# Optimization experiments

Hardware: AMD Instinct MI355X
Metric: run time of the kernel (lower is better)

Reference implementation:

```python
import jax, jax.numpy as jnp
import numpy as np


def _eta(pos, conj):
    # e[0] = pos[:,1::2] repeated into even/odd cols; e[1] = (+/-)pos[:,0::2] likewise
    c = jnp.repeat(pos[:, 1::2], 2, axis=1)
    s = jnp.repeat(pos[:, 0::2], 2, axis=1)
    return jnp.stack([c, s if conj else -s])  # [2, N, d]


def setup_inputs() -> dict:
    key = jax.random.key(0)
    ks = jax.random.split(key, 8)
    B, N, d, H = 8, 4096, 128, 4
    s = 0.02
    return {
        "x": jax.random.normal(ks[0], (B, N, d), jnp.float32),
        "pos": jax.random.normal(ks[1], (N, d), jnp.float32),
        "W_lt": jax.random.normal(ks[2], (d, d), jnp.float32) * s,
        "W_phi": jax.random.normal(ks[3], (d * H, d), jnp.float32) * s,
        "b_phi": jnp.zeros((d * H,), jnp.float32),
        "W_c1": jax.random.normal(ks[4], (H, H), jnp.float32) * s,
        "b_c1": jnp.zeros((H,), jnp.float32),
        "W_c2": jax.random.normal(ks[5], (1, H), jnp.float32) * s,
        "b_c2": jnp.zeros((1,), jnp.float32),
        "ln_g": jnp.ones((d,), jnp.float32),
        "ln_b": jnp.zeros((d,), jnp.float32),
        "W_f1": jax.random.normal(ks[6], (d, d), jnp.float32) * s,
        "b_f1": jnp.zeros((d,), jnp.float32),
        "W_f2": jax.random.normal(ks[7], (d, d), jnp.float32) * s,
        "b_f2": jnp.zeros((d,), jnp.float32),
    }


def reference(x, pos, W_lt, W_phi, b_phi, W_c1, b_c1, W_c2, b_c2,
              ln_g, ln_b, W_f1, b_f1, W_f2, b_f2):
    B, N, d = x.shape
    H = W_phi.shape[0] // d
    x = x @ W_lt.T                                   # linear_trans (no bias)
    e = _eta(pos, False)                             # [2,N,d]
    xe = x[None] * e[:, None]                        # [2,B,N,d]
    # A = ones(N,N) - I  =>  A @ v == sum over nodes minus self
    f = xe.sum(axis=2, keepdims=True) - xe           # [2,B,N,d]
    f_norm = jnp.sqrt(f[0] ** 2 + f[1] ** 2)         # [B,N,d]
    phi = ((x + pos[None]) @ W_phi.T + b_phi).reshape(B, N, H, d)
    # ReLU1(|f| - phi): relu(min(1, f_norm - phi))
    res = jax.nn.relu(jnp.minimum(1.0, f_norm[:, :, None, :] - phi))  # [B,N,H,d]
    ce = _eta(pos, True)
    fec = f[0] * ce[0][None] - f[1] * ce[1][None]    # [B,N,d]
    rfe = res * fec[:, :, None, :]                   # [B,N,H,d]
    # inverse transform: (1/N) * (M @ A) with A symmetric => sum-minus-self over node dim
    inv = (rfe.sum(axis=1, keepdims=True) - rfe) / N  # [B,N,H,d]
    t = inv.transpose(0, 1, 3, 2)                    # [B,N,d,H]
    comb = (jax.nn.relu(t @ W_c1.T + b_c1) @ W_c2.T + b_c2)[..., 0]  # [B,N,d]
    m = x + comb
    mu = m.mean(-1, keepdims=True)
    var = ((m - mu) ** 2).mean(-1, keepdims=True)
    mn = (m - mu) * jax.lax.rsqrt(var + 1e-6) * ln_g + ln_b
    return jax.nn.relu(mn @ W_f1.T + b_f1) @ W_f2.T + b_f2
```

## Files before the change

### kernel.cpp

```cpp
#include <hip/hip_runtime.h>
#include <hip/hip_bf16.h>


#define DEV __device__ __forceinline__

typedef __attribute__((ext_vector_type(8))) short bf16x8;
typedef __attribute__((ext_vector_type(4))) float f32x4;

constexpr int Bb = 8, Nn = 4096;
constexpr int BN = Bb * Nn;
constexpr int LDP = 136;
constexpr int P8  = 144;

union U8 { ushort u[8]; uint4 v; };

static DEV ushort f2bf(float f) {
    __hip_bfloat16 h = __float2bfloat16(f);
    return *reinterpret_cast<unsigned short*>(&h);
}
static DEV float bf2f(ushort u) {
    return __bfloat162float(*reinterpret_cast<const __hip_bfloat16*>(&u));
}
static DEV unsigned char f2fp8(float f) {
    return (unsigned char)(__builtin_amdgcn_cvt_pk_fp8_f32(f, f, 0u, false) & 0xff);
}
static DEV float fp8lo(unsigned int u, int) ;

__global__ __launch_bounds__(256) void k_gemm0(
    const float* __restrict__ X, const float* __restrict__ W,
    const float* __restrict__ pos, ushort* __restrict__ x1b,
    float* __restrict__ PS)
{
    __shared__ __align__(16) ushort xs[64 * LDP];
    __shared__ __align__(16) ushort wsl[128 * LDP];
    __shared__ float red[4][2][128];
    const int t = threadIdx.x;
    const int row0 = blockIdx.x * 64;

    #pragma unroll
    for (int i = 0; i < 4; ++i) {
        int e = t + i * 256, r = e >> 4, c = (e & 15) * 8;
        const float* p = X + (size_t)(row0 + r) * 128 + c;
        float4 a = *reinterpret_cast<const float4*>(p);
        float4 b = *reinterpret_cast<const float4*>(p + 4);
        U8 u;
        u.u[0] = f2bf(a.x); u.u[1] = f2bf(a.y); u.u[2] = f2bf(a.z); u.u[3] = f2bf(a.w);
        u.u[4] = f2bf(b.x); u.u[5] = f2bf(b.y); u.u[6] = f2bf(b.z); u.u[7] = f2bf(b.w);
        *reinterpret_cast<uint4*>(xs + r * LDP + c) = u.v;
    }
    #pragma unroll
    for (int i = 0; i < 8; ++i) {
        int e = t + i * 256, r = e >> 4, c = (e & 15) * 8;
        const float* p = W + (size_t)r * 128 + c;
        float4 a = *reinterpret_cast<const float4*>(p);
        float4 b = *reinterpret_cast<const float4*>(p + 4);
        U8 u;
        u.u[0] = f2bf(a.x); u.u[1] = f2bf(a.y); u.u[2] = f2bf(a.z); u.u[3] = f2bf(a.w);
        u.u[4] = f2bf(b.x); u.u[5] = f2bf(b.y); u.u[6] = f2bf(b.z); u.u[7] = f2bf(b.w);
        *reinterpret_cast<uint4*>(wsl + r * LDP + c) = u.v;
    }
    __syncthreads();

    const int w = t >> 6, l = t & 63;
    const int lr = l & 15;
    const int lk = (l >> 4) * 8;

    f32x4 acc[8];
    #pragma unroll
    for (int cf = 0; cf < 8; ++cf) acc[cf] = f32x4{0.f, 0.f, 0.f, 0.f};
    #pragma unroll
    for (int ks = 0; ks < 4; ++ks) {
        bf16x8 a = *reinterpret_cast<const bf16x8*>(xs + (w * 16 + lr) * LDP + ks * 32 + lk);
        #pragma unroll
        for (int cf = 0; cf < 8; ++cf) {
            bf16x8 b = *reinterpret_cast<const bf16x8*>(wsl + (cf * 16 + lr) * LDP + ks * 32 + lk);
            acc[cf] = __builtin_amdgcn_mfma_f32_16x16x32_bf16(a, b, acc[cf], 0, 0, 0);
        }
    }
    __syncthreads();

    #pragma unroll
    for (int cf = 0; cf < 8; ++cf) {
        int col = cf * 16 + lr;
        #pragma unroll
        for (int reg = 0; reg < 4; ++reg) {
            int rl = w * 16 + (l >> 4) * 4 + reg;
            xs[rl * LDP + col] = f2bf(acc[cf][reg]);
        }
    }
    __syncthreads();

    #pragma unroll
    for (int i = 0; i < 4; ++i) {
        int e = t + i * 256, r = e >> 4, c = (e & 15) * 8;
        uint4 v = *reinterpret_cast<const uint4*>(xs + r * LDP + c);
        *reinterpret_cast<uint4*>(x1b + (size_t)(row0 + r) * 128 + c) = v;
    }

    {
        int c2 = t & 63, g = t >> 6;
        float a0e = 0.f, a1e = 0.f, a0o = 0.f, a1o = 0.f;
        #pragma unroll 4
        for (int i = 0; i < 16; ++i) {
            int r = g * 16 + i;
            int n = (row0 + r) & (Nn - 1);
            unsigned int v = *reinterpret_cast<const unsigned int*>(xs + r * LDP + 2 * c2);
            float lo = bf2f((ushort)(v & 0xffff));
            float hi = bf2f((ushort)(v >> 16));
            float2 p = *reinterpret_cast<const float2*>(pos + (size_t)n * 128 + 2 * c2);
            a0e += lo * p.y; a1e += lo * p.x;
            a0o += hi * p.y; a1o += hi * p.x;
        }
        red[g][0][2 * c2] = a0e; red[g][0][2 * c2 + 1] = a0o;
        red[g][1][2 * c2] = a1e; red[g][1][2 * c2 + 1] = a1o;
    }
    __syncthreads();
    {
        int half = t >> 7, col = t & 127;
        float s = red[0][half][col] + red[1][half][col] + red[2][half][col] + red[3][half][col];
        PS[(size_t)blockIdx.x * 256 + t] = s;
    }
}

__global__ __launch_bounds__(256) void k_finS(
    const float* __restrict__ PS, float* __restrict__ S0, float* __restrict__ S1)
{
    int b = blockIdx.x, t = threadIdx.x;
    float s = 0.f;
    #pragma unroll 8
    for (int c = 0; c < 64; ++c) s += PS[(size_t)(b * 64 + c) * 256 + t];
    if (t < 128) S0[b * 128 + t] = s;
    else         S1[b * 128 + (t - 128)] = s;
}

__global__ __launch_bounds__(256) void k_gemm_phi(
    const ushort* __restrict__ x1b, const float* __restrict__ W,
    const float* __restrict__ bias, const float* __restrict__ pos,
    unsigned char* __restrict__ phi8)
{
    __shared__ __align__(16) ushort xs[64 * LDP];
    __shared__ __align__(16) ushort wsl[128 * LDP];
    __shared__ __align__(16) unsigned char p8[64 * P8];
    const int t = threadIdx.x;
    const int row0 = blockIdx.x * 64;
    const int w = t >> 6, l = t & 63;
    const int lr = l & 15;
    const int lk = (l >> 4) * 8;

    #pragma unroll
    for (int i = 0; i < 4; ++i) {
        int e = t + i * 256, r = e >> 4, c = (e & 15) * 8;
        U8 u;
        u.v = *reinterpret_cast<const uint4*>(x1b + (size_t)(row0 + r) * 128 + c);
        int n = (row0 + r) & (Nn - 1);
        const float* q = pos + (size_t)n * 128 + c;
        float4 pa = *reinterpret_cast<const float4*>(q);
        float4 pb = *reinterpret_cast<const float4*>(q + 4);
        u.u[0] = f2bf(bf2f(u.u[0]) + pa.x);
        u.u[1] = f2bf(bf2f(u.u[1]) + pa.y);
        u.u[2] = f2bf(bf2f(u.u[2]) + pa.z);
        u.u[3] = f2bf(bf2f(u.u[3]) + pa.w);
        u.u[4] = f2bf(bf2f(u.u[4]) + pb.x);
        u.u[5] = f2bf(bf2f(u.u[5]) + pb.y);
        u.u[6] = f2bf(bf2f(u.u[6]) + pb.z);
        u.u[7] = f2bf(bf2f(u.u[7]) + pb.w);
        *reinterpret_cast<uint4*>(xs + r * LDP + c) = u.v;
    }

    for (int jt = 0; jt < 4; ++jt) {
        __syncthreads();
        {
            const float* Wt = W + (size_t)jt * 128 * 128;
            #pragma unroll
            for (int i = 0; i < 8; ++i) {
                int e = t + i * 256, r = e >> 4, c = (e & 15) * 8;
                const float* p = Wt + (size_t)r * 128 + c;
                float4 a = *reinterpret_cast<const float4*>(p);
                float4 b = *reinterpret_cast<const float4*>(p + 4);
                U8 u;
                u.u[0] = f2bf(a.x); u.u[1] = f2bf(a.y); u.u[2] = f2bf(a.z); u.u[3] = f2bf(a.w);
                u.u[4] = f2bf(b.x); u.u[5] = f2bf(b.y); u.u[6] = f2bf(b.z); u.u[7] = f2bf(b.w);
                *reinterpret_cast<uint4*>(wsl + r * LDP + c) = u.v;
            }
            if (jt > 0) {
                #pragma unroll
                for (int i = 0; i < 2; ++i) {
                    int e = t + i * 256, r = e >> 3, c = (e & 7) * 16;
                    uint4 v = *reinterpret_cast<const uint4*>(p8 + r * P8 + c);
                    *reinterpret_cast<uint4*>(phi8 + (size_t)(row0 + r) * 512 + (jt - 1) * 128 + c) = v;
                }
            }
        }
        __syncthreads();

        f32x4 acc[8];
        #pragma unroll
        for (int cf = 0; cf < 8; ++cf) acc[cf] = f32x4{0.f, 0.f, 0.f, 0.f};
        #pragma unroll
        for (int ks = 0; ks < 4; ++ks) {
            bf16x8 a = *reinterpret_cast<const bf16x8*>(xs + (w * 16 + lr) * LDP + ks * 32 + lk);
            #pragma unroll
            for (int cf = 0; cf < 8; ++cf) {
                bf16x8 b = *reinterpret_cast<const bf16x8*>(wsl + (cf * 16 + lr) * LDP + ks * 32 + lk);
                acc[cf] = __builtin_amdgcn_mfma_f32_16x16x32_bf16(a, b, acc[cf], 0, 0, 0);
            }
        }
        #pragma unroll
        for (int cf = 0; cf < 8; ++cf) {
            int col = cf * 16 + lr;
            float bv = bias[jt * 128 + col];
            #pragma unroll
            for (int reg = 0; reg < 4; ++reg) {
                int rl = w * 16 + (l >> 4) * 4 + reg;
                p8[rl * P8 + col] = f2fp8(acc[cf][reg] + bv);
            }
        }
    }
    __syncthreads();
    #pragma unroll
    for (int i = 0; i < 2; ++i) {
        int e = t + i * 256, r = e >> 3, c = (e & 7) * 16;
        uint4 v = *reinterpret_cast<const uint4*>(p8 + r * P8 + c);
        *reinterpret_cast<uint4*>(phi8 + (size_t)(row0 + r) * 512 + 3 * 128 + c) = v;
    }
}

__global__ __launch_bounds__(256) void k_reduceT(
    const ushort* __restrict__ x1b, const unsigned char* __restrict__ phi8,
    const float* __restrict__ pos, const float* __restrict__ S0,
    const float* __restrict__ S1, float* __restrict__ PT)
{
    int b = blockIdx.x >> 6, c64 = blockIdx.x & 63;
    int rr = threadIdx.x >> 5, d0 = (threadIdx.x & 31) * 4;
    float4 S0v = *reinterpret_cast<const float4*>(S0 + b * 128 + d0);
    float4 S1v = *reinterpret_cast<const float4*>(S1 + b * 128 + d0);
    float S0a[4] = {S0v.x, S0v.y, S0v.z, S0v.w};
    float S1a[4] = {S1v.x, S1v.y, S1v.z, S1v.w};
    float acc[4][4];
    #pragma unroll
    for (int h = 0; h < 4; ++h)
        #pragma unroll
        for (int j = 0; j < 4; ++j) acc[h][j] = 0.f;

    #pragma unroll 2
    for (int i = 0; i < 8; ++i) {
        int n = c64 * 64 + i * 8 + rr;
        size_t r = (size_t)b * Nn + n;
        ushort4 xv4 = *reinterpret_cast<const ushort4*>(x1b + r * 128 + d0);
        float4 p = *reinterpret_cast<const float4*>(pos + (size_t)n * 128 + d0);
        float xv[4] = {bf2f(xv4.x), bf2f(xv4.y), bf2f(xv4.z), bf2f(xv4.w)};
        float cc[4] = {p.y, p.y, p.w, p.w};
        float ss[4] = {p.x, p.x, p.z, p.z};
        float fec[4], fn[4];
        #pragma unroll
        for (int j = 0; j < 4; ++j) {
            float f0 = S0a[j] - xv[j] * cc[j];
            float f1 = xv[j] * ss[j] - S1a[j];
            fn[j] = sqrtf(f0 * f0 + f1 * f1);
            fec[j] = f0 * cc[j] - f1 * ss[j];
        }
        #pragma unroll
        for (int h = 0; h < 4; ++h) {
            unsigned int pv = *reinterpret_cast<const unsigned int*>(phi8 + r * 512 + h * 128 + d0);
            float ph0 = __builtin_amdgcn_cvt_f32_fp8(pv, 0);
            float ph1 = __builtin_amdgcn_cvt_f32_fp8(pv, 1);
            float ph2 = __builtin_amdgcn_cvt_f32_fp8(pv, 2);
            float ph3 = __builtin_amdgcn_cvt_f32_fp8(pv, 3);
            acc[h][0] += fmaxf(0.f, fminf(1.f, fn[0] - ph0)) * fec[0];
            acc[h][1] += fmaxf(0.f, fminf(1.f, fn[1] - ph1)) * fec[1];
            acc[h][2] += fmaxf(0.f, fminf(1.f, fn[2] - ph2)) * fec[2];
            acc[h][3] += fmaxf(0.f, fminf(1.f, fn[3] - ph3)) * fec[3];
        }
    }
    __shared__ float red[8][512];
    #pragma unroll
    for (int h = 0; h < 4; ++h)
        #pragma unroll
        for (int j = 0; j < 4; ++j) red[rr][h * 128 + d0 + j] = acc[h][j];
    __syncthreads();
    int tt = threadIdx.x;
    #pragma unroll
    for (int q = 0; q < 2; ++q) {
        int idx = tt + q * 256;
        float s = 0.f;
        #pragma unroll
        for (int k = 0; k < 8; ++k) s += red[k][idx];
        PT[(size_t)blockIdx.x * 512 + idx] = s;
    }
}

__global__ __launch_bounds__(256) void k_finT(
    const float* __restrict__ PT, float* __restrict__ T)
{
    int idx = blockIdx.x * 256 + threadIdx.x;
    int b = idx >> 9, lo = idx & 511;
    float s = 0.f;
    #pragma unroll 8
    for (int c = 0; c < 64; ++c) s += PT[(size_t)b * 32768 + c * 512 + lo];
    T[idx] = s;
}

__global__ __launch_bounds__(256) void k_comb_ffn(
    const ushort* __restrict__ x1b, const unsigned char* __restrict__ phi8,
    const float* __restrict__ pos, const float* __restrict__ S0,
    const float* __restrict__ S1, const float* __restrict__ T,
    const float* __restrict__ Wc1, const float* __restrict__ bc1,
    const float* __restrict__ Wc2, const float* __restrict__ bc2,
    const float* __restrict__ lng, const float* __restrict__ lnb,
    const float* __restrict__ Wf1, const float* __restrict__ bf1,
    const float* __restrict__ Wf2, const float* __restrict__ bf2,
    float* __restrict__ out)
{
    __shared__ __align__(16) ushort xs[64 * LDP];
    __shared__ __align__(16) ushort wsl[128 * LDP];
    const int t = threadIdx.x;
    const int row0 = blockIdx.x * 64;
    const int w = t >> 6, l = t & 63;

    #pragma unroll
    for (int i = 0; i < 8; ++i) {
        int e = t + i * 256, r = e >> 4, c = (e & 15) * 8;
        const float* p = Wf1 + (size_t)r * 128 + c;
        float4 a = *reinterpret_cast<const float4*>(p);
        float4 b = *reinterpret_cast<const float4*>(p + 4);
        U8 u;
        u.u[0] = f2bf(a.x); u.u[1] = f2bf(a.y); u.u[2] = f2bf(a.z); u.u[3] = f2bf(a.w);
        u.u[4] = f2bf(b.x); u.u[5] = f2bf(b.y); u.u[6] = f2bf(b.z); u.u[7] = f2bf(b.w);
        *reinterpret_cast<uint4*>(wsl + r * LDP + c) = u.v;
    }

    {
        const int d0 = 2 * l;
        const float g0 = lng[d0], g1 = lng[d0 + 1];
        const float be0 = lnb[d0], be1 = lnb[d0 + 1];
        const float c2v[4] = {Wc2[0], Wc2[1], Wc2[2], Wc2[3]};
        const float b2v = bc2[0];
        for (int i = 0; i < 16; ++i) {
            int rl = w * 16 + i;
            int rrow = row0 + rl;
            int b = rrow >> 12;
            int n = rrow & 4095;
            size_t r = (size_t)rrow;

            ushort2 xv2 = *reinterpret_cast<const ushort2*>(x1b + r * 128 + d0);
            float2 p2 = *reinterpret_cast<const float2*>(pos + (size_t)n * 128 + d0);
            float2 s0 = *reinterpret_cast<const float2*>(S0 + b * 128 + d0);
            float2 s1 = *reinterpret_cast<const float2*>(S1 + b * 128 + d0);
            float cc = p2.y, ss = p2.x;
            float xv[2] = {bf2f(xv2.x), bf2f(xv2.y)};
            float S0a[2] = {s0.x, s0.y}, S1a[2] = {s1.x, s1.y};
            float2 Tv[4];
            #pragma unroll
            for (int h = 0; h < 4; ++h)
                Tv[h] = *reinterpret_cast<const float2*>(T + (b * 4 + h) * 128 + d0);
            float phv[4][2];
            #pragma unroll
            for (int h = 0; h < 4; ++h) {
                unsigned int pu = *reinterpret_cast<const ushort*>(phi8 + r * 512 + h * 128 + d0);
                phv[h][0] = __builtin_amdgcn_cvt_f32_fp8(pu, 0);
                phv[h][1] = __builtin_amdgcn_cvt_f32_fp8(pu, 1);
            }

            float m[2];
            #pragma unroll
            for (int q = 0; q < 2; ++q) {
                float f0 = S0a[q] - xv[q] * cc;
                float f1 = xv[q] * ss - S1a[q];
                float fn = sqrtf(f0 * f0 + f1 * f1);
                float fec = f0 * cc - f1 * ss;
                float inv[4];
                #pragma unroll
                for (int h = 0; h < 4; ++h) {
                    float res = fmaxf(0.f, fminf(1.f, fn - phv[h][q]));
                    float tv = q ? Tv[h].y : Tv[h].x;
                    inv[h] = (tv - res * fec) * (1.f / (float)Nn);
                }
                float comb = b2v;
                #pragma unroll
                for (int h = 0; h < 4; ++h) {
                    float u = bc1[h];
                    #pragma unroll
                    for (int h2 = 0; h2 < 4; ++h2) u += Wc1[h * 4 + h2] * inv[h2];
                    comb += fmaxf(u, 0.f) * c2v[h];
                }
                m[q] = xv[q] + comb;
            }

            float s = m[0] + m[1];
            #pragma unroll
            for (int off = 32; off; off >>= 1) s += __shfl_xor(s, off);
            float mu = s * (1.f / 128.f);
            float e0 = m[0] - mu, e1 = m[1] - mu;
            float v = e0 * e0 + e1 * e1;
            #pragma unroll
            for (int off = 32; off; off >>= 1) v += __shfl_xor(v, off);
            float rstd = rsqrtf(v * (1.f / 128.f) + 1e-6f);
            ushort2 o;
            o.x = f2bf(e0 * rstd * g0 + be0);
            o.y = f2bf(e1 * rstd * g1 + be1);
            *reinterpret_cast<ushort2*>(xs + rl * LDP + d0) = o;
        }
    }
    __syncthreads();

    const int lr = l & 15;
    const int lk = (l >> 4) * 8;

    f32x4 acc[8];
    #pragma unroll
    for (int cf = 0; cf < 8; ++cf) acc[cf] = f32x4{0.f, 0.f, 0.f, 0.f};
    #pragma unroll
    for (int ks = 0; ks < 4; ++ks) {
        bf16x8 a = *reinterpret_cast<const bf16x8*>(xs + (w * 16 + lr) * LDP + ks * 32 + lk);
        #pragma unroll
        for (int cf = 0; cf < 8; ++cf) {
            bf16x8 b = *reinterpret_cast<const bf16x8*>(wsl + (cf * 16 + lr) * LDP + ks * 32 + lk);
            acc[cf] = __builtin_amdgcn_mfma_f32_16x16x32_bf16(a, b, acc[cf], 0, 0, 0);
        }
    }
    __syncthreads();

    #pragma unroll
    for (int cf = 0; cf < 8; ++cf) {
        int col = cf * 16 + lr;
        float bv = bf1[col];
        #pragma unroll
        for (int reg = 0; reg < 4; ++reg) {
            int rl = w * 16 + (l >> 4) * 4 + reg;
            xs[rl * LDP + col] = f2bf(fmaxf(acc[cf][reg] + bv, 0.f));
        }
    }
    #pragma unroll
    for (int i = 0; i < 8; ++i) {
        int e = t + i * 256, r = e >> 4, c = (e & 15) * 8;
        const float* p = Wf2 + (size_t)r * 128 + c;
        float4 a = *reinterpret_cast<const float4*>(p);
        float4 b = *reinterpret_cast<const float4*>(p + 4);
        U8 u;
        u.u[0] = f2bf(a.x); u.u[1] = f2bf(a.y); u.u[2] = f2bf(a.z); u.u[3] = f2bf(a.w);
        u.u[4] = f2bf(b.x); u.u[5] = f2bf(b.y); u.u[6] = f2bf(b.z); u.u[7] = f2bf(b.w);
        *reinterpret_cast<uint4*>(wsl + r * LDP + c) = u.v;
    }
    __syncthreads();

    #pragma unroll
    for (int cf = 0; cf < 8; ++cf) acc[cf] = f32x4{0.f, 0.f, 0.f, 0.f};
    #pragma unroll
    for (int ks = 0; ks < 4; ++ks) {
        bf16x8 a = *reinterpret_cast<const bf16x8*>(xs + (w * 16 + lr) * LDP + ks * 32 + lk);
        #pragma unroll
        for (int cf = 0; cf < 8; ++cf) {
            bf16x8 b = *reinterpret_cast<const bf16x8*>(wsl + (cf * 16 + lr) * LDP + ks * 32 + lk);
            acc[cf] = __builtin_amdgcn_mfma_f32_16x16x32_bf16(a, b, acc[cf], 0, 0, 0);
        }
    }
    #pragma unroll
    for (int cf = 0; cf < 8; ++cf) {
        int col = cf * 16 + lr;
        float bv = bf2[col];
        #pragma unroll
        for (int reg = 0; reg < 4; ++reg) {
            int r = row0 + w * 16 + (l >> 4) * 4 + reg;
            out[(size_t)r * 128 + col] = acc[cf][reg] + bv;
        }
    }
}

extern "C" void kernel_launch(void* const* d_in, const int* in_sizes, int n_in,
                              void* d_out, int out_size, void* d_ws, size_t ws_size,
                              hipStream_t stream)
{
    const float* x    = (const float*)d_in[0];
    const float* pos  = (const float*)d_in[1];
    const float* Wlt  = (const float*)d_in[2];
    const float* Wphi = (const float*)d_in[3];
    const float* bphi = (const float*)d_in[4];
    const float* Wc1  = (const float*)d_in[5];
    const float* bc1  = (const float*)d_in[6];
    const float* Wc2  = (const float*)d_in[7];
    const float* bc2  = (const float*)d_in[8];
    const float* lng  = (const float*)d_in[9];
    const float* lnb  = (const float*)d_in[10];
    const float* Wf1  = (const float*)d_in[11];
    const float* bf1  = (const float*)d_in[12];
    const float* Wf2  = (const float*)d_in[13];
    const float* bf2  = (const float*)d_in[14];

    float* ws = (float*)d_ws;
    ushort* x1b = (ushort*)ws;
    float* S0   = ws + 2097152;
    float* S1   = S0 + 1024;
    float* T    = S1 + 1024;
    float* PS   = T + 4096;
    float* PT   = PS + 131072;
    unsigned char* phi8 = (unsigned char*)(ws + 2496512);
    float* out  = (float*)d_out;

    k_gemm0<<<dim3(BN / 64), 256, 0, stream>>>(x, Wlt, pos, x1b, PS);
    k_finS<<<dim3(Bb), 256, 0, stream>>>(PS, S0, S1);
    k_gemm_phi<<<dim3(BN / 64), 256, 0, stream>>>(x1b, Wphi, bphi, pos, phi8);
    k_reduceT<<<dim3(512), 256, 0, stream>>>(x1b, phi8, pos, S0, S1, PT);
    k_finT<<<dim3(16), 256, 0, stream>>>(PT, T);
    k_comb_ffn<<<dim3(BN / 64), 256, 0, stream>>>(x1b, phi8, pos, S0, S1, T,
                                                  Wc1, bc1, Wc2, bc2, lng, lnb,
                                                  Wf1, bf1, Wf2, bf2, out);
}
```

Baseline: 72.65 us.

## Fuse S/T finalize and T-reduction into neighbouring GEMM kernels, cutting launches

The small finalize kernels for S and T are folded into their consumers: each phi block recomputes the per-batch S sum from partials, and each comb block reduces the T partials into shared memory. The T partial reduction is moved into the phi GEMM kernel so it runs right after each fp8 phi tile is written, which avoids re-reading phi8 and x1b from global memory. This goes from six launches to three at the cost of redundant partial-sum reductions in every block. It also changes the x input to the reduction: xs there holds x1+pos in bf16 and pos is subtracted back, which adds rounding error.

```diff
diff --git a/kernel.cpp b/kernel.cpp
--- a/kernel.cpp
+++ b/kernel.cpp
@@ -24,10 +24,9 @@
 static DEV unsigned char f2fp8(float f) {
     return (unsigned char)(__builtin_amdgcn_cvt_pk_fp8_f32(f, f, 0u, false) & 0xff);
 }
-static DEV float fp8lo(unsigned int u, int) ;
-
-__global__ __launch_bounds__(256) void k_gemm0(
-    const float* __restrict__ X, const float* __restrict__ W,
+
+__global__ __launch_bounds__(256) void k_gemmS(
+    const float* __restrict__ X, const float* __restrict__ Wlt,
     const float* __restrict__ pos, ushort* __restrict__ x1b,
     float* __restrict__ PS)
 {
@@ -36,6 +35,9 @@
     __shared__ float red[4][2][128];
     const int t = threadIdx.x;
     const int row0 = blockIdx.x * 64;
+    const int w = t >> 6, l = t & 63;
+    const int lr = l & 15;
+    const int lk = (l >> 4) * 8;
 
     #pragma unroll
     for (int i = 0; i < 4; ++i) {
@@ -51,7 +53,7 @@
     #pragma unroll
     for (int i = 0; i < 8; ++i) {
         int e = t + i * 256, r = e >> 4, c = (e & 15) * 8;
-        const float* p = W + (size_t)r * 128 + c;
+        const float* p = Wlt + (size_t)r * 128 + c;
         float4 a = *reinterpret_cast<const float4*>(p);
         float4 b = *reinterpret_cast<const float4*>(p + 4);
         U8 u;
@@ -61,10 +63,6 @@
     }
     __syncthreads();
 
-    const int w = t >> 6, l = t & 63;
-    const int lr = l & 15;
-    const int lk = (l >> 4) * 8;
-
     f32x4 acc[8];
     #pragma unroll
     for (int cf = 0; cf < 8; ++cf) acc[cf] = f32x4{0.f, 0.f, 0.f, 0.f};
@@ -96,7 +94,6 @@
         uint4 v = *reinterpret_cast<const uint4*>(xs + r * LDP + c);
         *reinterpret_cast<uint4*>(x1b + (size_t)(row0 + r) * 128 + c) = v;
     }
-
     {
         int c2 = t & 63, g = t >> 6;
         float a0e = 0.f, a1e = 0.f, a0o = 0.f, a1o = 0.f;
@@ -122,31 +119,38 @@
     }
 }
 
-__global__ __launch_bounds__(256) void k_finS(
-    const float* __restrict__ PS, float* __restrict__ S0, float* __restrict__ S1)
-{
-    int b = blockIdx.x, t = threadIdx.x;
-    float s = 0.f;
-    #pragma unroll 8
-    for (int c = 0; c < 64; ++c) s += PS[(size_t)(b * 64 + c) * 256 + t];
-    if (t < 128) S0[b * 128 + t] = s;
-    else         S1[b * 128 + (t - 128)] = s;
-}
-
-__global__ __launch_bounds__(256) void k_gemm_phi(
-    const ushort* __restrict__ x1b, const float* __restrict__ W,
-    const float* __restrict__ bias, const float* __restrict__ pos,
-    unsigned char* __restrict__ phi8)
+__global__ __launch_bounds__(256) void k_phiT(
+    const ushort* __restrict__ x1b, const float* __restrict__ Wphi,
+    const float* __restrict__ bphi, const float* __restrict__ pos,
+    const float* __restrict__ PS, float* __restrict__ S0,
+    float* __restrict__ S1, unsigned char* __restrict__ phi8,
+    float* __restrict__ PT)
 {
     __shared__ __align__(16) ushort xs[64 * LDP];
     __shared__ __align__(16) ushort wsl[128 * LDP];
     __shared__ __align__(16) unsigned char p8[64 * P8];
+    __shared__ float Sld[256];
+    __shared__ float red[4][512];
     const int t = threadIdx.x;
+    const int b = blockIdx.x >> 6;
+    const int c64 = blockIdx.x & 63;
     const int row0 = blockIdx.x * 64;
     const int w = t >> 6, l = t & 63;
     const int lr = l & 15;
     const int lk = (l >> 4) * 8;
-
+    const int c2 = t & 63, g = t >> 6;
+
+    {
+        const float* base = PS + (size_t)b * 64 * 256 + t;
+        float s = 0.f;
+        #pragma unroll 8
+        for (int c = 0; c < 64; ++c) s += base[c * 256];
+        Sld[t] = s;
+        if (c64 == 0) {
+            if (t < 128) S0[b * 128 + t] = s;
+            else         S1[b * 128 + (t - 128)] = s;
+        }
+    }
     #pragma unroll
     for (int i = 0; i < 4; ++i) {
         int e = t + i * 256, r = e >> 4, c = (e & 15) * 8;
@@ -166,144 +170,117 @@
         u.u[7] = f2bf(bf2f(u.u[7]) + pb.w);
         *reinterpret_cast<uint4*>(xs + r * LDP + c) = u.v;
     }
+    #pragma unroll
+    for (int i = 0; i < 8; ++i) {
+        int e = t + i * 256, r = e >> 4, c = (e & 15) * 8;
+        const float* p = Wphi + (size_t)r * 128 + c;
+        float4 a = *reinterpret_cast<const float4*>(p);
+        float4 bq = *reinterpret_cast<const float4*>(p + 4);
+        U8 u;
+        u.u[0] = f2bf(a.x); u.u[1] = f2bf(a.y); u.u[2] = f2bf(a.z); u.u[3] = f2bf(a.w);
+        u.u[4] = f2bf(bq.x); u.u[5] = f2bf(bq.y); u.u[6] = f2bf(bq.z); u.u[7] = f2bf(bq.w);
+        *reinterpret_cast<uint4*>(wsl + r * LDP + c) = u.v;
+    }
+    __syncthreads();
+
+    float tp[4][2];
+    #pragma unroll
+    for (int jt = 0; jt < 4; ++jt) { tp[jt][0] = 0.f; tp[jt][1] = 0.f; }
+
+    const float S0e = Sld[2 * c2],       S0o = Sld[2 * c2 + 1];
+    const float S1e = Sld[128 + 2 * c2], S1o = Sld[128 + 2 * c2 + 1];
 
     for (int jt = 0; jt < 4; ++jt) {
+        f32x4 acc[8];
+        #pragma unroll
+        for (int cf = 0; cf < 8; ++cf) acc[cf] = f32x4{0.f, 0.f, 0.f, 0.f};
+        #pragma unroll
+        for (int ks = 0; ks < 4; ++ks) {
+            bf16x8 a = *reinterpret_cast<const bf16x8*>(xs + (w * 16 + lr) * LDP + ks * 32 + lk);
+            #pragma unroll
+            for (int cf = 0; cf < 8; ++cf) {
+                bf16x8 bb = *reinterpret_cast<const bf16x8*>(wsl + (cf * 16 + lr) * LDP + ks * 32 + lk);
+                acc[cf] = __builtin_amdgcn_mfma_f32_16x16x32_bf16(a, bb, acc[cf], 0, 0, 0);
+            }
+        }
+        #pragma unroll
+        for (int cf = 0; cf < 8; ++cf) {
+            int col = cf * 16 + lr;
+            float bv = bphi[jt * 128 + col];
+            #pragma unroll
+            for (int reg = 0; reg < 4; ++reg) {
+                int rl = w * 16 + (l >> 4) * 4 + reg;
+                p8[rl * P8 + col] = f2fp8(acc[cf][reg] + bv);
+            }
+        }
         __syncthreads();
+
+        #pragma unroll
+        for (int i = 0; i < 2; ++i) {
+            int e = t + i * 256, r = e >> 3, c = (e & 7) * 16;
+            uint4 v = *reinterpret_cast<const uint4*>(p8 + r * P8 + c);
+            *reinterpret_cast<uint4*>(phi8 + (size_t)(row0 + r) * 512 + jt * 128 + c) = v;
+        }
         {
-            const float* Wt = W + (size_t)jt * 128 * 128;
+            float acc0 = 0.f, acc1 = 0.f;
+            #pragma unroll 4
+            for (int i = 0; i < 16; ++i) {
+                int r = g * 16 + i;
+                int n = (row0 + r) & (Nn - 1);
+                float2 p = *reinterpret_cast<const float2*>(pos + (size_t)n * 128 + 2 * c2);
+                unsigned int xv = *reinterpret_cast<const unsigned int*>(xs + r * LDP + 2 * c2);
+                float xe = bf2f((ushort)(xv & 0xffff)) - p.x;
+                float xo = bf2f((ushort)(xv >> 16)) - p.y;
+                float f0e = S0e - xe * p.y, f1e = xe * p.x - S1e;
+                float f0o = S0o - xo * p.y, f1o = xo * p.x - S1o;
+                float fne = sqrtf(f0e * f0e + f1e * f1e);
+                float fno = sqrtf(f0o * f0o + f1o * f1o);
+                float fece = f0e * p.y - f1e * p.x;
+                float feco = f0o * p.y - f1o * p.x;
+                unsigned int pu = *reinterpret_cast<const ushort*>(p8 + r * P8 + 2 * c2);
+                float phe = __builtin_amdgcn_cvt_f32_fp8(pu, 0);
+                float pho = __builtin_amdgcn_cvt_f32_fp8(pu, 1);
+                acc0 += fmaxf(0.f, fminf(1.f, fne - phe)) * fece;
+                acc1 += fmaxf(0.f, fminf(1.f, fno - pho)) * feco;
+            }
+            tp[jt][0] = acc0;
+            tp[jt][1] = acc1;
+        }
+        if (jt < 3) {
+            const float* Wt = Wphi + (size_t)(jt + 1) * 128 * 128;
             #pragma unroll
             for (int i = 0; i < 8; ++i) {
                 int e = t + i * 256, r = e >> 4, c = (e & 15) * 8;
                 const float* p = Wt + (size_t)r * 128 + c;
                 float4 a = *reinterpret_cast<const float4*>(p);
-                float4 b = *reinterpret_cast<const float4*>(p + 4);
+                float4 bq = *reinterpret_cast<const float4*>(p + 4);
                 U8 u;
                 u.u[0] = f2bf(a.x); u.u[1] = f2bf(a.y); u.u[2] = f2bf(a.z); u.u[3] = f2bf(a.w);
-                u.u[4] = f2bf(b.x); u.u[5] = f2bf(b.y); u.u[6] = f2bf(b.z); u.u[7] = f2bf(b.w);
+                u.u[4] = f2bf(bq.x); u.u[5] = f2bf(bq.y); u.u[6] = f2bf(bq.z); u.u[7] = f2bf(bq.w);
                 *reinterpret_cast<uint4*>(wsl + r * LDP + c) = u.v;
             }
-            if (jt > 0) {
-                #pragma unroll
-                for (int i = 0; i < 2; ++i) {
-                    int e = t + i * 256, r = e >> 3, c = (e & 7) * 16;
-                    uint4 v = *reinterpret_cast<const uint4*>(p8 + r * P8 + c);
-                    *reinterpret_cast<uint4*>(phi8 + (size_t)(row0 + r) * 512 + (jt - 1) * 128 + c) = v;
-                }
-            }
         }
         __syncthreads();
-
-        f32x4 acc[8];
-        #pragma unroll
-        for (int cf = 0; cf < 8; ++cf) acc[cf] = f32x4{0.f, 0.f, 0.f, 0.f};
-        #pragma unroll
-        for (int ks = 0; ks < 4; ++ks) {
-            bf16x8 a = *reinterpret_cast<const bf16x8*>(xs + (w * 16 + lr) * LDP + ks * 32 + lk);
-            #pragma unroll
-            for (int cf = 0; cf < 8; ++cf) {
-                bf16x8 b = *reinterpret_cast<const bf16x8*>(wsl + (cf * 16 + lr) * LDP + ks * 32 + lk);
-                acc[cf] = __builtin_amdgcn_mfma_f32_16x16x32_bf16(a, b, acc[cf], 0, 0, 0);
-            }
-        }
-        #pragma unroll
-        for (int cf = 0; cf < 8; ++cf) {
-            int col = cf * 16 + lr;
-            float bv = bias[jt * 128 + col];
-            #pragma unroll
-            for (int reg = 0; reg < 4; ++reg) {
-                int rl = w * 16 + (l >> 4) * 4 + reg;
-                p8[rl * P8 + col] = f2fp8(acc[cf][reg] + bv);
-            }
-        }
-    }
-    __syncthreads();
-    #pragma unroll
-    for (int i = 0; i < 2; ++i) {
-        int e = t + i * 256, r = e >> 3, c = (e & 7) * 16;
-        uint4 v = *reinterpret_cast<const uint4*>(p8 + r * P8 + c);
-        *reinterpret_cast<uint4*>(phi8 + (size_t)(row0 + r) * 512 + 3 * 128 + c) = v;
-    }
-}
-
-__global__ __launch_bounds__(256) void k_reduceT(
-    const ushort* __restrict__ x1b, const unsigned char* __restrict__ phi8,
-    const float* __restrict__ pos, const float* __restrict__ S0,
-    const float* __restrict__ S1, float* __restrict__ PT)
-{
-    int b = blockIdx.x >> 6, c64 = blockIdx.x & 63;
-    int rr = threadIdx.x >> 5, d0 = (threadIdx.x & 31) * 4;
-    float4 S0v = *reinterpret_cast<const float4*>(S0 + b * 128 + d0);
-    float4 S1v = *reinterpret_cast<const float4*>(S1 + b * 128 + d0);
-    float S0a[4] = {S0v.x, S0v.y, S0v.z, S0v.w};
-    float S1a[4] = {S1v.x, S1v.y, S1v.z, S1v.w};
-    float acc[4][4];
-    #pragma unroll
-    for (int h = 0; h < 4; ++h)
-        #pragma unroll
-        for (int j = 0; j < 4; ++j) acc[h][j] = 0.f;
-
-    #pragma unroll 2
-    for (int i = 0; i < 8; ++i) {
-        int n = c64 * 64 + i * 8 + rr;
-        size_t r = (size_t)b * Nn + n;
-        ushort4 xv4 = *reinterpret_cast<const ushort4*>(x1b + r * 128 + d0);
-        float4 p = *reinterpret_cast<const float4*>(pos + (size_t)n * 128 + d0);
-        float xv[4] = {bf2f(xv4.x), bf2f(xv4.y), bf2f(xv4.z), bf2f(xv4.w)};
-        float cc[4] = {p.y, p.y, p.w, p.w};
-        float ss[4] = {p.x, p.x, p.z, p.z};
-        float fec[4], fn[4];
-        #pragma unroll
-        for (int j = 0; j < 4; ++j) {
-            float f0 = S0a[j] - xv[j] * cc[j];
-            float f1 = xv[j] * ss[j] - S1a[j];
-            fn[j] = sqrtf(f0 * f0 + f1 * f1);
-            fec[j] = f0 * cc[j] - f1 * ss[j];
-        }
-        #pragma unroll
-        for (int h = 0; h < 4; ++h) {
-            unsigned int pv = *reinterpret_cast<const unsigned int*>(phi8 + r * 512 + h * 128 + d0);
-            float ph0 = __builtin_amdgcn_cvt_f32_fp8(pv, 0);
-            float ph1 = __builtin_amdgcn_cvt_f32_fp8(pv, 1);
-            float ph2 = __builtin_amdgcn_cvt_f32_fp8(pv, 2);
-            float ph3 = __builtin_amdgcn_cvt_f32_fp8(pv, 3);
-            acc[h][0] += fmaxf(0.f, fminf(1.f, fn[0] - ph0)) * fec[0];
-            acc[h][1] += fmaxf(0.f, fminf(1.f, fn[1] - ph1)) * fec[1];
-            acc[h][2] += fmaxf(0.f, fminf(1.f, fn[2] - ph2)) * fec[2];
-            acc[h][3] += fmaxf(0.f, fminf(1.f, fn[3] - ph3)) * fec[3];
-        }
-    }
-    __shared__ float red[8][512];
-    #pragma unroll
-    for (int h = 0; h < 4; ++h)
-        #pragma unroll
-        for (int j = 0; j < 4; ++j) red[rr][h * 128 + d0 + j] = acc[h][j];
-    __syncthreads();
-    int tt = threadIdx.x;
+    }
+
+    #pragma unroll
+    for (int jt = 0; jt < 4; ++jt) {
+        red[g][jt * 128 + 2 * c2] = tp[jt][0];
+        red[g][jt * 128 + 2 * c2 + 1] = tp[jt][1];
+    }
+    __syncthreads();
     #pragma unroll
     for (int q = 0; q < 2; ++q) {
-        int idx = tt + q * 256;
-        float s = 0.f;
-        #pragma unroll
-        for (int k = 0; k < 8; ++k) s += red[k][idx];
+        int idx = t + q * 256;
+        float s = red[0][idx] + red[1][idx] + red[2][idx] + red[3][idx];
         PT[(size_t)blockIdx.x * 512 + idx] = s;
     }
-}
-
-__global__ __launch_bounds__(256) void k_finT(
-    const float* __restrict__ PT, float* __restrict__ T)
-{
-    int idx = blockIdx.x * 256 + threadIdx.x;
-    int b = idx >> 9, lo = idx & 511;
-    float s = 0.f;
-    #pragma unroll 8
-    for (int c = 0; c < 64; ++c) s += PT[(size_t)b * 32768 + c * 512 + lo];
-    T[idx] = s;
 }
 
 __global__ __launch_bounds__(256) void k_comb_ffn(
     const ushort* __restrict__ x1b, const unsigned char* __restrict__ phi8,
     const float* __restrict__ pos, const float* __restrict__ S0,
-    const float* __restrict__ S1, const float* __restrict__ T,
+    const float* __restrict__ S1, const float* __restrict__ PT,
     const float* __restrict__ Wc1, const float* __restrict__ bc1,
     const float* __restrict__ Wc2, const float* __restrict__ bc2,
     const float* __restrict__ lng, const float* __restrict__ lnb,
@@ -313,10 +290,23 @@
 {
     __shared__ __align__(16) ushort xs[64 * LDP];
     __shared__ __align__(16) ushort wsl[128 * LDP];
+    __shared__ float Tld[512];
     const int t = threadIdx.x;
     const int row0 = blockIdx.x * 64;
     const int w = t >> 6, l = t & 63;
-
+    const int bb = row0 >> 12;
+
+    {
+        const float* base = PT + (size_t)bb * 64 * 512;
+        #pragma unroll
+        for (int q = 0; q < 2; ++q) {
+            int idx = t + q * 256;
+            float s = 0.f;
+            #pragma unroll 8
+            for (int c = 0; c < 64; ++c) s += base[c * 512 + idx];
+            Tld[idx] = s;
+        }
+    }
     #pragma unroll
     for (int i = 0; i < 8; ++i) {
         int e = t + i * 256, r = e >> 4, c = (e & 15) * 8;
@@ -328,6 +318,7 @@
         u.u[4] = f2bf(b.x); u.u[5] = f2bf(b.y); u.u[6] = f2bf(b.z); u.u[7] = f2bf(b.w);
         *reinterpret_cast<uint4*>(wsl + r * LDP + c) = u.v;
     }
+    __syncthreads();
 
     {
         const int d0 = 2 * l;
@@ -335,24 +326,23 @@
         const float be0 = lnb[d0], be1 = lnb[d0 + 1];
         const float c2v[4] = {Wc2[0], Wc2[1], Wc2[2], Wc2[3]};
         const float b2v = bc2[0];
+        float2 s0 = *reinterpret_cast<const float2*>(S0 + bb * 128 + d0);
+        float2 s1 = *reinterpret_cast<const float2*>(S1 + bb * 128 + d0);
+        float S0a[2] = {s0.x, s0.y}, S1a[2] = {s1.x, s1.y};
+        float Tv[4][2];
+        #pragma unroll
+        for (int h = 0; h < 4; ++h) { Tv[h][0] = Tld[h * 128 + d0]; Tv[h][1] = Tld[h * 128 + d0 + 1]; }
+
         for (int i = 0; i < 16; ++i) {
             int rl = w * 16 + i;
             int rrow = row0 + rl;
-            int b = rrow >> 12;
             int n = rrow & 4095;
             size_t r = (size_t)rrow;
 
             ushort2 xv2 = *reinterpret_cast<const ushort2*>(x1b + r * 128 + d0);
             float2 p2 = *reinterpret_cast<const float2*>(pos + (size_t)n * 128 + d0);
-            float2 s0 = *reinterpret_cast<const float2*>(S0 + b * 128 + d0);
-            float2 s1 = *reinterpret_cast<const float2*>(S1 + b * 128 + d0);
             float cc = p2.y, ss = p2.x;
             float xv[2] = {bf2f(xv2.x), bf2f(xv2.y)};
-            float S0a[2] = {s0.x, s0.y}, S1a[2] = {s1.x, s1.y};
-            float2 Tv[4];
-            #pragma unroll
-            for (int h = 0; h < 4; ++h)
-                Tv[h] = *reinterpret_cast<const float2*>(T + (b * 4 + h) * 128 + d0);
             float phv[4][2];
             #pragma unroll
             for (int h = 0; h < 4; ++h) {
@@ -372,8 +362,7 @@
                 #pragma unroll
                 for (int h = 0; h < 4; ++h) {
                     float res = fmaxf(0.f, fminf(1.f, fn - phv[h][q]));
-                    float tv = q ? Tv[h].y : Tv[h].x;
-                    inv[h] = (tv - res * fec) * (1.f / (float)Nn);
+                    inv[h] = (Tv[h][q] - res * fec) * (1.f / (float)Nn);
                 }
                 float comb = b2v;
                 #pragma unroll
@@ -490,18 +479,14 @@
     ushort* x1b = (ushort*)ws;
     float* S0   = ws + 2097152;
     float* S1   = S0 + 1024;
-    float* T    = S1 + 1024;
-    float* PS   = T + 4096;
+    float* PS   = S1 + 1024;
     float* PT   = PS + 131072;
-    unsigned char* phi8 = (unsigned char*)(ws + 2496512);
+    unsigned char* phi8 = (unsigned char*)(ws + 2492416);
     float* out  = (float*)d_out;
 
-    k_gemm0<<<dim3(BN / 64), 256, 0, stream>>>(x, Wlt, pos, x1b, PS);
-    k_finS<<<dim3(Bb), 256, 0, stream>>>(PS, S0, S1);
-    k_gemm_phi<<<dim3(BN / 64), 256, 0, stream>>>(x1b, Wphi, bphi, pos, phi8);
-    k_reduceT<<<dim3(512), 256, 0, stream>>>(x1b, phi8, pos, S0, S1, PT);
-    k_finT<<<dim3(16), 256, 0, stream>>>(PT, T);
-    k_comb_ffn<<<dim3(BN / 64), 256, 0, stream>>>(x1b, phi8, pos, S0, S1, T,
+    k_gemmS<<<dim3(BN / 64), 256, 0, stream>>>(x, Wlt, pos, x1b, PS);
+    k_phiT<<<dim3(BN / 64), 256, 0, stream>>>(x1b, Wphi, bphi, pos, PS, S0, S1, phi8, PT);
+    k_comb_ffn<<<dim3(BN / 64), 256, 0, stream>>>(x1b, phi8, pos, S0, S1, PT,
                                                   Wc1, bc1, Wc2, bc2, lng, lnb,
                                                   Wf1, bf1, Wf2, bf2, out);
 }
```

Measured after the change: 76.46 us. 1.05x slower.
